# Performance work log

Hardware: AMD Instinct MI355X
Metric: run time of the kernel (lower is better)

## Reference

```python
import jax, jax.numpy as jnp
import numpy as np
import math

D_MODEL, N_HEADS, D_FF = 1024, 16, 4096
HEAD_DIM = D_MODEL // N_HEADS
BATCH, SEQ = 2, 2048
POPE_BASE = 10000.0
LN_EPS = 1e-5


def setup_inputs() -> dict:
    key = jax.random.key(0)
    ks = jax.random.split(key, 20)
    s = 0.02
    inp = {
        "x": jax.random.normal(ks[0], (BATCH, SEQ, D_MODEL), dtype=jnp.float32),
        "positions": jnp.arange(SEQ, dtype=jnp.int64) if jax.config.jax_enable_x64 else jnp.arange(SEQ, dtype=jnp.int32),
        "Wq": jax.random.normal(ks[1], (D_MODEL, D_MODEL), jnp.float32) * s,
        "bq": jnp.zeros((D_MODEL,), jnp.float32),
        "Wk": jax.random.normal(ks[2], (D_MODEL, D_MODEL), jnp.float32) * s,
        "bk": jnp.zeros((D_MODEL,), jnp.float32),
        "Wv": jax.random.normal(ks[3], (D_MODEL, D_MODEL), jnp.float32) * s,
        "bv": jnp.zeros((D_MODEL,), jnp.float32),
        "Wo": jax.random.normal(ks[4], (D_MODEL, D_MODEL), jnp.float32) * s,
        "bo": jnp.zeros((D_MODEL,), jnp.float32),
        "phase_bias": jax.random.uniform(ks[5], (N_HEADS, HEAD_DIM), jnp.float32,
                                          minval=-2.0 * math.pi, maxval=0.0),
        "freqs": (1.0 / POPE_BASE ** (jnp.arange(HEAD_DIM, dtype=jnp.float32) / HEAD_DIM)),
        "W1": jax.random.normal(ks[6], (D_MODEL, D_FF), jnp.float32) * s,
        "b1": jnp.zeros((D_FF,), jnp.float32),
        "W2": jax.random.normal(ks[7], (D_FF, D_MODEL), jnp.float32) * s,
        "b2": jnp.zeros((D_MODEL,), jnp.float32),
        "g1": jnp.ones((D_MODEL,), jnp.float32),
        "beta1": jnp.zeros((D_MODEL,), jnp.float32),
        "g2": jnp.ones((D_MODEL,), jnp.float32),
        "beta2": jnp.zeros((D_MODEL,), jnp.float32),
    }
    return inp


def _layernorm(x, g, b):
    mu = jnp.mean(x, axis=-1, keepdims=True)
    var = jnp.mean((x - mu) ** 2, axis=-1, keepdims=True)
    return (x - mu) * jax.lax.rsqrt(var + LN_EPS) * g + b


def reference(x, positions, Wq, bq, Wk, bk, Wv, bv, Wo, bo, phase_bias, freqs,
              W1, b1, W2, b2, g1, beta1, g2, beta2):
    B, S, D = x.shape
    H, hd = N_HEADS, HEAD_DIM

    def split_heads(y):  # (B,S,D) -> (B,H,S,hd)
        return y.reshape(B, S, H, hd).transpose(0, 2, 1, 3)

    q = split_heads(x @ Wq + bq)
    k = split_heads(x @ Wk + bk)
    v = split_heads(x @ Wv + bv)

    # --- PoPE: magnitudes via softplus, phases from positions + learned bias ---
    mu_q = jax.nn.softplus(q)
    mu_k = jax.nn.softplus(k)
    pos_phases = positions[:, None].astype(jnp.float32) * freqs[None, :]        # (S,hd)
    phases = pos_phases[None, None, :, :] + phase_bias[None, :, None, :]        # (1,H,S,hd)
    cosp, sinp = jnp.cos(phases), jnp.sin(phases)
    q_pope = jnp.concatenate([mu_q * cosp, mu_q * sinp], axis=-1)               # (B,H,S,2hd)
    k_pope = jnp.concatenate([mu_k * cosp, mu_k * sinp], axis=-1)

    # --- manual causal attention with softmax1 ---
    scale = 1.0 / math.sqrt(2 * hd)  # q.shape[-1] == 2*head_dim under PoPE
    scores = jnp.einsum("bhsd,bhtd->bhst", q_pope, k_pope) * scale
    causal = jnp.triu(jnp.ones((S, S), dtype=bool), k=1)
    scores = jnp.where(causal[None, None], -jnp.inf, scores)
    m = jnp.max(scores, axis=-1, keepdims=True)
    e = jnp.exp(scores - m)
    attn_w = e / (1.0 + jnp.sum(e, axis=-1, keepdims=True))  # softmax1 (as written in source)
    attn = jnp.einsum("bhst,bhtd->bhsd", attn_w, v)

    attn = attn.transpose(0, 2, 1, 3).reshape(B, S, D) @ Wo + bo
    x = _layernorm(x + attn, g1, beta1)
    ff = jax.nn.relu(x @ W1 + b1) @ W2 + b2
    x = _layernorm(x + ff, g2, beta2)
    return x
```

## Files before the change

kernel.cpp:

```cpp
#include <hip/hip_runtime.h>
#include <hip/hip_bf16.h>
#include <math.h>

#define B_   2
#define S_   2048
#define D_   1024
#define H_   16
#define HD_  64
#define DFF_ 4096
#define M_   (B_*S_)
#define SCALE_ 0.08838834764831845f

typedef __attribute__((ext_vector_type(8))) short bf16x8;
typedef __attribute__((ext_vector_type(4))) float f32x4;

#define MFMA16(a,b,c) __builtin_amdgcn_mfma_f32_16x16x32_bf16((a),(b),(c),0,0,0)

__device__ __forceinline__ unsigned short f2b(float f) {
    union { float f; unsigned u; } v; v.f = f;
    return (unsigned short)((v.u + 0x7FFFu + ((v.u >> 16) & 1u)) >> 16);
}
__device__ __forceinline__ float b2f(unsigned short s) {
    union { unsigned u; float f; } v; v.u = ((unsigned)s) << 16;
    return v.f;
}
__device__ __forceinline__ unsigned pk2bf(float a, float b) {
    union { float f; unsigned u; } ua, ub; ua.f = a; ub.f = b;
    return __builtin_amdgcn_perm(ub.u, ua.u, 0x07060302u);
}
__device__ __forceinline__ float softplus_f(float x) {
    return fmaxf(x, 0.f) + log1pf(__expf(-fabsf(x)));
}
__device__ __forceinline__ void g2l16(const void* g, void* l) {
    __builtin_amdgcn_global_load_lds(
        (const __attribute__((address_space(1))) unsigned int*)g,
        (__attribute__((address_space(3))) unsigned int*)l, 16, 0, 0);
}

__global__ __launch_bounds__(256) void conv_bf16_kernel(
    const float* __restrict__ in, unsigned short* __restrict__ out)
{
    int i = blockIdx.x * 256 + threadIdx.x;
    out[i] = f2b(in[i]);
}

__global__ __launch_bounds__(256) void wtrans_kernel(
    const float* __restrict__ W, unsigned short* __restrict__ WT, int K, int N)
{
    __shared__ float tile[32][33];
    const int n0 = blockIdx.x * 32, k0 = blockIdx.y * 32;
    const int tx = threadIdx.x & 31, ty = threadIdx.x >> 5;
    #pragma unroll
    for (int i = 0; i < 4; i++)
        tile[ty + 8*i][tx] = W[(size_t)(k0 + ty + 8*i) * N + n0 + tx];
    __syncthreads();
    #pragma unroll
    for (int i = 0; i < 4; i++)
        WT[(size_t)(n0 + ty + 8*i) * K + k0 + tx] = f2b(tile[tx][ty + 8*i]);
}

__global__ __launch_bounds__(256) void bcat_kernel(
    const float* __restrict__ a, const float* __restrict__ b,
    const float* __restrict__ c, float* __restrict__ o)
{
    int i = blockIdx.x * 256 + threadIdx.x;
    o[i] = (i < 1024) ? a[i] : (i < 2048 ? b[i - 1024] : c[i - 2048]);
}

__global__ __launch_bounds__(256) void gemm_bf16_kernel(
    const unsigned short* __restrict__ A,
    const unsigned short* __restrict__ WT,
    const float* __restrict__ bias,
    float* __restrict__ outF, unsigned short* __restrict__ outB,
    int M, int Kslice, int lda, int N, int relu)
{
    __shared__ unsigned short As[128 * 64];
    __shared__ unsigned short Bs[128 * 64];

    const int tid = threadIdx.x;
    const int w = tid >> 6, lane = tid & 63;
    const int quad = lane >> 4, l16 = lane & 15;
    const size_t m0 = (size_t)blockIdx.y * 128, n0 = (size_t)blockIdx.x * 128;
    const int wm = (w >> 1) * 64, wn = (w & 1) * 64;
    const int koff = blockIdx.z * Kslice;

    const int srow = lane >> 3;
    const int sc   = ((lane & 7) ^ srow) * 8;
    const unsigned short* ga = A  + (m0 + w * 32 + srow) * (size_t)lda + koff + sc;
    const unsigned short* gb = WT + (n0 + w * 32 + srow) * (size_t)lda + koff + sc;
    const size_t rows8 = (size_t)8 * lda;

    f32x4 acc[4][4] = {};

    for (int k0 = 0; k0 < Kslice; k0 += 64) {
        #pragma unroll
        for (int j = 0; j < 4; j++)
            g2l16(ga + j * rows8 + k0, &As[(w * 32 + j * 8) * 64]);
        #pragma unroll
        for (int j = 0; j < 4; j++)
            g2l16(gb + j * rows8 + k0, &Bs[(w * 32 + j * 8) * 64]);
        __syncthreads();

        #pragma unroll
        for (int kk = 0; kk < 2; kk++) {
            bf16x8 af[4], bfr[4];
            #pragma unroll
            for (int t = 0; t < 4; t++) {
                const int slot = ((kk * 4 + quad) ^ (l16 & 7)) * 8;
                af[t]  = *(const bf16x8*)&As[(wm + t * 16 + l16) * 64 + slot];
                bfr[t] = *(const bf16x8*)&Bs[(wn + t * 16 + l16) * 64 + slot];
            }
            #pragma unroll
            for (int mt = 0; mt < 4; mt++)
                #pragma unroll
                for (int nt = 0; nt < 4; nt++)
                    acc[mt][nt] = MFMA16(af[mt], bfr[nt], acc[mt][nt]);
        }
        __syncthreads();
    }

    float bv[4];
    #pragma unroll
    for (int nt = 0; nt < 4; nt++)
        bv[nt] = (blockIdx.z == 0) ? bias[n0 + wn + nt * 16 + l16] : 0.f;

    float* outFz = outF ? outF + (size_t)blockIdx.z * M * N : nullptr;

    #pragma unroll
    for (int mt = 0; mt < 4; mt++) {
        #pragma unroll
        for (int nt = 0; nt < 4; nt++) {
            const size_t n = n0 + wn + nt * 16 + l16;
            #pragma unroll
            for (int r = 0; r < 4; r++) {
                const size_t m = m0 + wm + mt * 16 + quad * 4 + r;
                float val = acc[mt][nt][r] + bv[nt];
                if (relu) val = fmaxf(val, 0.f);
                const size_t idx = m * N + n;
                if (outFz) outFz[idx] = val;
                if (outB) outB[idx] = f2b(val);
            }
        }
    }
}

__global__ __launch_bounds__(256) void pope_kernel(
    const unsigned short* __restrict__ qkv,
    const float* __restrict__ phase_bias, const float* __restrict__ freqs,
    unsigned short* __restrict__ qp, unsigned short* __restrict__ kp)
{
    int idx = blockIdx.x * 256 + threadIdx.x;
    int d = idx & 63;
    int s = (idx >> 6) & (S_ - 1);
    int h = (idx >> 17) & (H_ - 1);
    int b = idx >> 21;

    size_t src = (size_t)(b * S_ + s) * 3072 + h * HD_ + d;
    float muq = softplus_f(b2f(qkv[src])) * SCALE_;
    float muk = softplus_f(b2f(qkv[src + 1024]));

    float ph = (float)s * freqs[d] + phase_bias[h * HD_ + d];
    float sn, cs;
    sincosf(ph, &sn, &cs);

    size_t o = ((size_t)(b * H_ + h) * S_ + s) * 128 + d;
    qp[o]      = f2b(muq * cs);
    qp[o + 64] = f2b(muq * sn);
    kp[o]      = f2b(muk * cs);
    kp[o + 64] = f2b(muk * sn);
}

__global__ __launch_bounds__(256) void vtrans_kernel(
    const unsigned short* __restrict__ qkv, unsigned short* __restrict__ vt)
{
    __shared__ unsigned short tile[64][72];
    const int bh = blockIdx.y, b = bh >> 4, h = bh & 15;
    const int s0 = blockIdx.x * 64;
    const int tid = threadIdx.x;
    #pragma unroll
    for (int i = 0; i < 16; i++) {
        int idx = i * 256 + tid;
        int s = idx >> 6, d = idx & 63;
        tile[s][d] = qkv[(size_t)(b * S_ + s0 + s) * 3072 + 2048 + h * HD_ + d];
    }
    __syncthreads();
    #pragma unroll
    for (int i = 0; i < 16; i++) {
        int idx = i * 256 + tid;
        int d = idx >> 6, s = idx & 63;
        vt[((size_t)bh * 64 + d) * S_ + s0 + s] = tile[s][d];
    }
}

__global__ __launch_bounds__(512, 4) void attn_mfma_kernel(
    const unsigned short* __restrict__ qp,
    const unsigned short* __restrict__ kp,
    const unsigned short* __restrict__ vt,
    unsigned short* __restrict__ ao)
{
    __shared__ unsigned short kt_lds[2][64][128];
    __shared__ unsigned short vt_lds[2][64][64];
    __shared__ unsigned short p_lds[8][16][72];

    const int tid = threadIdx.x;
    const int w = tid >> 6, lane = tid & 63;
    const int quad = lane >> 4, l16 = lane & 15;
    const int bh = blockIdx.y, b = bh >> 4, h = bh & 15;

    const int a = (blockIdx.z == 0) ? 15 - (int)blockIdx.x : (int)blockIdx.x;
    const int q0b = a * 128;
    const int q0 = q0b + w * 16;

    const unsigned short* qbase = qp + ((size_t)bh * S_ + q0 + l16) * 128 + quad * 8;
    bf16x8 qa[4];
    #pragma unroll
    for (int kc = 0; kc < 4; kc++) qa[kc] = *(const bf16x8*)(qbase + kc * 32);

    const int krow = lane >> 4, kslot = lane & 15;
    const int vrow = lane >> 3, vslot = lane & 7;
    const int kr0 = w * 8 + krow,     kc0 = kslot ^ (kr0 & 15);
    const int kr1 = w * 8 + 4 + krow, kc1 = kslot ^ (kr1 & 15);
    const int vd  = w * 8 + vrow,     vc  = vslot ^ (vd & 7);
    const unsigned short* kg0 = kp + ((size_t)bh * S_ + kr0) * 128 + kc0 * 8;
    const unsigned short* kg1 = kp + ((size_t)bh * S_ + kr1) * 128 + kc1 * 8;
    const unsigned short* vg0 = vt + ((size_t)bh * 64 + vd) * S_ + vc * 8;

    f32x4 o[4] = {};
    float ms = -1e30f, ls = 0.f;

    const int ntiles = 2 * a + 2;

    g2l16(kg0, &kt_lds[0][w * 8][0]);
    g2l16(kg1, &kt_lds[0][w * 8 + 4][0]);
    g2l16(vg0, &vt_lds[0][w * 8][0]);

    for (int ti = 0; ti < ntiles; ti++) {
        const int t0 = ti * 64;
        __syncthreads();
        if (ti + 1 < ntiles) {
            const int nb = (ti + 1) & 1;
            const size_t ko = (size_t)(ti + 1) * (64 * 128);
            const size_t vo = (size_t)(ti + 1) * 64;
            g2l16(kg0 + ko, &kt_lds[nb][w * 8][0]);
            g2l16(kg1 + ko, &kt_lds[nb][w * 8 + 4][0]);
            g2l16(vg0 + vo, &vt_lds[nb][w * 8][0]);
        }
        const int buf = ti & 1;

        if (t0 <= q0 + 15) {
            f32x4 sf[4];
            #pragma unroll
            for (int kg = 0; kg < 4; kg++) {
                f32x4 s = {0, 0, 0, 0};
                const int row = kg * 16 + l16;
                #pragma unroll
                for (int kc = 0; kc < 4; kc++) {
                    const int slot = (kc * 4 + quad) ^ l16;
                    s = MFMA16(*(const bf16x8*)&kt_lds[buf][row][slot * 8], qa[kc], s);
                }
                sf[kg] = s;
            }

            const int qrow = q0 + l16;
            const bool dmask = (t0 + 63 > q0);
            #pragma unroll
            for (int kg = 0; kg < 4; kg++) {
                const int kbase = t0 + kg * 16 + quad * 4;
                float v0 = sf[kg][0], v1 = sf[kg][1], v2 = sf[kg][2], v3 = sf[kg][3];
                if (dmask) {
                    v0 = (kbase     <= qrow) ? v0 : -1e30f;
                    v1 = (kbase + 1 <= qrow) ? v1 : -1e30f;
                    v2 = (kbase + 2 <= qrow) ? v2 : -1e30f;
                    v3 = (kbase + 3 <= qrow) ? v3 : -1e30f;
                }
                ms = fmaxf(ms, fmaxf(fmaxf(v0, v1), fmaxf(v2, v3)));
                const float e0 = __expf(v0), e1 = __expf(v1);
                const float e2 = __expf(v2), e3 = __expf(v3);
                ls += (e0 + e1) + (e2 + e3);
                uint2 pk;
                pk.x = pk2bf(e0, e1);
                pk.y = pk2bf(e2, e3);
                *(uint2*)&p_lds[w][l16][kg * 16 + quad * 4] = pk;
            }
            asm volatile("s_waitcnt lgkmcnt(0)" ::: "memory");
            bf16x8 pa0 = *(const bf16x8*)&p_lds[w][l16][quad * 8];
            bf16x8 pa1 = *(const bf16x8*)&p_lds[w][l16][quad * 8 + 32];

            #pragma unroll
            for (int dg = 0; dg < 4; dg++) {
                const int row = dg * 16 + l16;
                const int s0_ = quad ^ (l16 & 7);
                const int s1_ = (quad + 4) ^ (l16 & 7);
                o[dg] = MFMA16(pa0, *(const bf16x8*)&vt_lds[buf][row][s0_ * 8], o[dg]);
                o[dg] = MFMA16(pa1, *(const bf16x8*)&vt_lds[buf][row][s1_ * 8], o[dg]);
            }
        }
    }

    float mv = ms, lv = ls;
    mv = fmaxf(mv, __shfl_xor(mv, 16, 64)); lv += __shfl_xor(lv, 16, 64);
    mv = fmaxf(mv, __shfl_xor(mv, 32, 64)); lv += __shfl_xor(lv, 32, 64);
    const float inv = 1.f / (__expf(mv) + lv);

    #pragma unroll
    for (int r = 0; r < 4; r++) {
        const float ir = __shfl(inv, quad * 4 + r, 64);
        const int row = q0 + quad * 4 + r;
        const size_t base = (size_t)(b * S_ + row) * D_ + h * HD_ + l16;
        ao[base]      = f2b(o[0][r] * ir);
        ao[base + 16] = f2b(o[1][r] * ir);
        ao[base + 32] = f2b(o[2][r] * ir);
        ao[base + 48] = f2b(o[3][r] * ir);
    }
}

__global__ __launch_bounds__(256) void ln_kernel(
    const float* __restrict__ ya, const float* __restrict__ yb,
    const float* __restrict__ res,
    const float* __restrict__ g, const float* __restrict__ beta,
    float* __restrict__ out, unsigned short* __restrict__ outB)
{
    const int row = blockIdx.x;
    const int tid = threadIdx.x;
    const float* yr = ya + (size_t)row * D_;
    const float* y2 = yb ? yb + (size_t)row * D_ : nullptr;
    const float* rr = res + (size_t)row * D_;

    float t[4];
    float sum = 0.f, sumsq = 0.f;
    #pragma unroll
    for (int i = 0; i < 4; i++) {
        int c = tid + 256 * i;
        t[i] = yr[c] + rr[c] + (y2 ? y2[c] : 0.f);
        sum += t[i]; sumsq += t[i] * t[i];
    }
    #pragma unroll
    for (int off = 32; off >= 1; off >>= 1) {
        sum   += __shfl_xor(sum,   off, 64);
        sumsq += __shfl_xor(sumsq, off, 64);
    }
    __shared__ float rs_[4], rq_[4];
    int w = tid >> 6, lane = tid & 63;
    if (lane == 0) { rs_[w] = sum; rq_[w] = sumsq; }
    __syncthreads();
    float tot  = rs_[0] + rs_[1] + rs_[2] + rs_[3];
    float totq = rq_[0] + rq_[1] + rq_[2] + rq_[3];
    float mu   = tot  * (1.f / D_);
    float var  = totq * (1.f / D_) - mu * mu;
    float rstd = rsqrtf(var + 1e-5f);

    float* orow = out + (size_t)row * D_;
    #pragma unroll
    for (int i = 0; i < 4; i++) {
        int c = tid + 256 * i;
        float val = (t[i] - mu) * rstd * g[c] + beta[c];
        orow[c] = val;
        if (outB) outB[(size_t)row * D_ + c] = f2b(val);
    }
}

extern "C" void kernel_launch(void* const* d_in, const int* in_sizes, int n_in,
                              void* d_out, int out_size, void* d_ws, size_t ws_size,
                              hipStream_t stream)
{
    const float* x   = (const float*)d_in[0];
    const float* Wq  = (const float*)d_in[2];
    const float* bq  = (const float*)d_in[3];
    const float* Wk  = (const float*)d_in[4];
    const float* bk  = (const float*)d_in[5];
    const float* Wv  = (const float*)d_in[6];
    const float* bv  = (const float*)d_in[7];
    const float* Wo  = (const float*)d_in[8];
    const float* bo  = (const float*)d_in[9];
    const float* phase_bias = (const float*)d_in[10];
    const float* freqs = (const float*)d_in[11];
    const float* W1  = (const float*)d_in[12];
    const float* b1  = (const float*)d_in[13];
    const float* W2  = (const float*)d_in[14];
    const float* b2  = (const float*)d_in[15];
    const float* g1  = (const float*)d_in[16];
    const float* be1 = (const float*)d_in[17];
    const float* g2  = (const float*)d_in[18];
    const float* be2 = (const float*)d_in[19];
    float* out = (float*)d_out;

    char* base = (char*)d_ws;
    const size_t MiB = 1024 * 1024;
    unsigned short* WqkvT = (unsigned short*)(base);
    unsigned short* WoT   = (unsigned short*)(base + 6  * MiB);
    unsigned short* W1T   = (unsigned short*)(base + 8  * MiB);
    unsigned short* W2T   = (unsigned short*)(base + 16 * MiB);
    float*          bqkv  = (float*)(base + 24 * MiB);
    unsigned short* xb    = (unsigned short*)(base + 25 * MiB);
    unsigned short* qkvb  = (unsigned short*)(base + 33 * MiB);
    unsigned short* qpb   = (unsigned short*)(base + 57 * MiB);
    unsigned short* kpb   = (unsigned short*)(base + 73 * MiB);
    unsigned short* vtb   = (unsigned short*)(base + 89 * MiB);
    float*          po    = (float*)(base + 89 * MiB);
    float*          x1    = (float*)(base + 121 * MiB);
    unsigned short* aob   = xb;
    unsigned short* x1b   = xb;
    unsigned short* hb    = qkvb;
    float*          fo    = po;

    dim3 blk(256);

    conv_bf16_kernel<<<dim3(M_ * D_ / 256), blk, 0, stream>>>(x, xb);
    wtrans_kernel<<<dim3(32, 32), blk, 0, stream>>>(Wq, WqkvT, D_, D_);
    wtrans_kernel<<<dim3(32, 32), blk, 0, stream>>>(Wk, WqkvT + (size_t)1024 * 1024, D_, D_);
    wtrans_kernel<<<dim3(32, 32), blk, 0, stream>>>(Wv, WqkvT + (size_t)2048 * 1024, D_, D_);
    wtrans_kernel<<<dim3(32, 32), blk, 0, stream>>>(Wo, WoT, D_, D_);
    wtrans_kernel<<<dim3(DFF_ / 32, D_ / 32), blk, 0, stream>>>(W1, W1T, D_, DFF_);
    wtrans_kernel<<<dim3(D_ / 32, DFF_ / 32), blk, 0, stream>>>(W2, W2T, DFF_, D_);
    bcat_kernel<<<dim3(12), blk, 0, stream>>>(bq, bk, bv, bqkv);

    gemm_bf16_kernel<<<dim3(3072 / 128, M_ / 128, 1), blk, 0, stream>>>(
        xb, WqkvT, bqkv, nullptr, qkvb, M_, D_, D_, 3072, 0);

    pope_kernel<<<dim3(B_ * H_ * S_ * HD_ / 256), blk, 0, stream>>>(
        qkvb, phase_bias, freqs, qpb, kpb);
    vtrans_kernel<<<dim3(S_ / 64, B_ * H_), blk, 0, stream>>>(qkvb, vtb);

    attn_mfma_kernel<<<dim3(8, B_ * H_, 2), dim3(512), 0, stream>>>(qpb, kpb, vtb, aob);

    gemm_bf16_kernel<<<dim3(D_ / 128, M_ / 128, 2), blk, 0, stream>>>(
        aob, WoT, bo, po, nullptr, M_, D_ / 2, D_, D_, 0);
    ln_kernel<<<dim3(M_), blk, 0, stream>>>(po, po + (size_t)M_ * D_, x, g1, be1, x1, x1b);

    gemm_bf16_kernel<<<dim3(DFF_ / 128, M_ / 128, 1), blk, 0, stream>>>(
        x1b, W1T, b1, nullptr, hb, M_, D_, D_, DFF_, 1);
    gemm_bf16_kernel<<<dim3(D_ / 128, M_ / 128, 2), blk, 0, stream>>>(
        hb, W2T, b2, fo, nullptr, M_, DFF_ / 2, DFF_, D_, 0);
    ln_kernel<<<dim3(M_), blk, 0, stream>>>(fo, fo + (size_t)M_ * D_, x1, g2, be2, out, nullptr);
}
```

Baseline: 417.2 us.

## Double-buffer GEMM LDS tiles, remap blocks across XCDs, drop fp32 residual copy

The GEMM now prefetches the next K tile into a second LDS buffer while computing on the current one, with a single barrier per iteration. Block indices are remapped so consecutive tiles land on the same XCD for better L2 reuse. The input conversion kernel is vectorized to four elements per thread. The first layernorm writes only a bf16 output, and the second layernorm reads that as its residual. This removes one fp32 write and read, at the cost of residual precision and doubled LDS usage per block.

```diff
diff --git a/kernel.cpp b/kernel.cpp
--- a/kernel.cpp
+++ b/kernel.cpp
@@ -40,8 +40,11 @@
 __global__ __launch_bounds__(256) void conv_bf16_kernel(
     const float* __restrict__ in, unsigned short* __restrict__ out)
 {
-    int i = blockIdx.x * 256 + threadIdx.x;
-    out[i] = f2b(in[i]);
+    int i = (blockIdx.x * 256 + threadIdx.x) * 4;
+    float4 v = *(const float4*)&in[i];
+    ushort4 o;
+    o.x = f2b(v.x); o.y = f2b(v.y); o.z = f2b(v.z); o.w = f2b(v.w);
+    *(ushort4*)&out[i] = o;
 }
 
 __global__ __launch_bounds__(256) void wtrans_kernel(
@@ -74,15 +77,24 @@
     float* __restrict__ outF, unsigned short* __restrict__ outB,
     int M, int Kslice, int lda, int N, int relu)
 {
-    __shared__ unsigned short As[128 * 64];
-    __shared__ unsigned short Bs[128 * 64];
+    __shared__ unsigned short As[2][128 * 64];
+    __shared__ unsigned short Bs[2][128 * 64];
 
     const int tid = threadIdx.x;
     const int w = tid >> 6, lane = tid & 63;
     const int quad = lane >> 4, l16 = lane & 15;
-    const size_t m0 = (size_t)blockIdx.y * 128, n0 = (size_t)blockIdx.x * 128;
+
+    const int nn = gridDim.x, nm = gridDim.y;
+    const int lin = ((int)blockIdx.z * nm + (int)blockIdx.y) * nn + (int)blockIdx.x;
+    const int per = (nn * nm * (int)gridDim.z) >> 3;
+    const int id  = (lin & 7) * per + (lin >> 3);
+    const int zz  = id / (nn * nm);
+    const int rem = id - zz * nn * nm;
+    const int mt_ = rem / nn, nt_ = rem - mt_ * nn;
+
+    const size_t m0 = (size_t)mt_ * 128, n0 = (size_t)nt_ * 128;
     const int wm = (w >> 1) * 64, wn = (w & 1) * 64;
-    const int koff = blockIdx.z * Kslice;
+    const int koff = zz * Kslice;
 
     const int srow = lane >> 3;
     const int sc   = ((lane & 7) ^ srow) * 8;
@@ -91,15 +103,25 @@
     const size_t rows8 = (size_t)8 * lda;
 
     f32x4 acc[4][4] = {};
-
-    for (int k0 = 0; k0 < Kslice; k0 += 64) {
-        #pragma unroll
-        for (int j = 0; j < 4; j++)
-            g2l16(ga + j * rows8 + k0, &As[(w * 32 + j * 8) * 64]);
-        #pragma unroll
-        for (int j = 0; j < 4; j++)
-            g2l16(gb + j * rows8 + k0, &Bs[(w * 32 + j * 8) * 64]);
+    const int niter = Kslice >> 6;
+
+    #pragma unroll
+    for (int j = 0; j < 4; j++) g2l16(ga + j * rows8, &As[0][(w * 32 + j * 8) * 64]);
+    #pragma unroll
+    for (int j = 0; j < 4; j++) g2l16(gb + j * rows8, &Bs[0][(w * 32 + j * 8) * 64]);
+
+    for (int i = 0; i < niter; i++) {
         __syncthreads();
+        if (i + 1 < niter) {
+            const int nb = (i + 1) & 1, k0 = (i + 1) << 6;
+            #pragma unroll
+            for (int j = 0; j < 4; j++)
+                g2l16(ga + j * rows8 + k0, &As[nb][(w * 32 + j * 8) * 64]);
+            #pragma unroll
+            for (int j = 0; j < 4; j++)
+                g2l16(gb + j * rows8 + k0, &Bs[nb][(w * 32 + j * 8) * 64]);
+        }
+        const int buf = i & 1;
 
         #pragma unroll
         for (int kk = 0; kk < 2; kk++) {
@@ -107,8 +129,8 @@
             #pragma unroll
             for (int t = 0; t < 4; t++) {
                 const int slot = ((kk * 4 + quad) ^ (l16 & 7)) * 8;
-                af[t]  = *(const bf16x8*)&As[(wm + t * 16 + l16) * 64 + slot];
-                bfr[t] = *(const bf16x8*)&Bs[(wn + t * 16 + l16) * 64 + slot];
+                af[t]  = *(const bf16x8*)&As[buf][(wm + t * 16 + l16) * 64 + slot];
+                bfr[t] = *(const bf16x8*)&Bs[buf][(wn + t * 16 + l16) * 64 + slot];
             }
             #pragma unroll
             for (int mt = 0; mt < 4; mt++)
@@ -116,15 +138,14 @@
                 for (int nt = 0; nt < 4; nt++)
                     acc[mt][nt] = MFMA16(af[mt], bfr[nt], acc[mt][nt]);
         }
-        __syncthreads();
     }
 
     float bv[4];
     #pragma unroll
     for (int nt = 0; nt < 4; nt++)
-        bv[nt] = (blockIdx.z == 0) ? bias[n0 + wn + nt * 16 + l16] : 0.f;
-
-    float* outFz = outF ? outF + (size_t)blockIdx.z * M * N : nullptr;
+        bv[nt] = (zz == 0) ? bias[n0 + wn + nt * 16 + l16] : 0.f;
+
+    float* outFz = outF ? outF + (size_t)zz * M * N : nullptr;
 
     #pragma unroll
     for (int mt = 0; mt < 4; mt++) {
@@ -316,22 +337,22 @@
 
 __global__ __launch_bounds__(256) void ln_kernel(
     const float* __restrict__ ya, const float* __restrict__ yb,
-    const float* __restrict__ res,
+    const float* __restrict__ resF, const unsigned short* __restrict__ resB,
     const float* __restrict__ g, const float* __restrict__ beta,
-    float* __restrict__ out, unsigned short* __restrict__ outB)
+    float* __restrict__ outF, unsigned short* __restrict__ outB)
 {
     const int row = blockIdx.x;
     const int tid = threadIdx.x;
     const float* yr = ya + (size_t)row * D_;
     const float* y2 = yb ? yb + (size_t)row * D_ : nullptr;
-    const float* rr = res + (size_t)row * D_;
 
     float t[4];
     float sum = 0.f, sumsq = 0.f;
     #pragma unroll
     for (int i = 0; i < 4; i++) {
         int c = tid + 256 * i;
-        t[i] = yr[c] + rr[c] + (y2 ? y2[c] : 0.f);
+        float rv = resF ? resF[(size_t)row * D_ + c] : b2f(resB[(size_t)row * D_ + c]);
+        t[i] = yr[c] + rv + (y2 ? y2[c] : 0.f);
         sum += t[i]; sumsq += t[i] * t[i];
     }
     #pragma unroll
@@ -349,12 +370,11 @@
     float var  = totq * (1.f / D_) - mu * mu;
     float rstd = rsqrtf(var + 1e-5f);
 
-    float* orow = out + (size_t)row * D_;
     #pragma unroll
     for (int i = 0; i < 4; i++) {
         int c = tid + 256 * i;
         float val = (t[i] - mu) * rstd * g[c] + beta[c];
-        orow[c] = val;
+        if (outF) outF[(size_t)row * D_ + c] = val;
         if (outB) outB[(size_t)row * D_ + c] = f2b(val);
     }
 }
@@ -397,7 +417,6 @@
     unsigned short* kpb   = (unsigned short*)(base + 73 * MiB);
     unsigned short* vtb   = (unsigned short*)(base + 89 * MiB);
     float*          po    = (float*)(base + 89 * MiB);
-    float*          x1    = (float*)(base + 121 * MiB);
     unsigned short* aob   = xb;
     unsigned short* x1b   = xb;
     unsigned short* hb    = qkvb;
@@ -405,7 +424,7 @@
 
     dim3 blk(256);
 
-    conv_bf16_kernel<<<dim3(M_ * D_ / 256), blk, 0, stream>>>(x, xb);
+    conv_bf16_kernel<<<dim3(M_ * D_ / 1024), blk, 0, stream>>>(x, xb);
     wtrans_kernel<<<dim3(32, 32), blk, 0, stream>>>(Wq, WqkvT, D_, D_);
     wtrans_kernel<<<dim3(32, 32), blk, 0, stream>>>(Wk, WqkvT + (size_t)1024 * 1024, D_, D_);
     wtrans_kernel<<<dim3(32, 32), blk, 0, stream>>>(Wv, WqkvT + (size_t)2048 * 1024, D_, D_);
@@ -425,11 +444,13 @@
 
     gemm_bf16_kernel<<<dim3(D_ / 128, M_ / 128, 2), blk, 0, stream>>>(
         aob, WoT, bo, po, nullptr, M_, D_ / 2, D_, D_, 0);
-    ln_kernel<<<dim3(M_), blk, 0, stream>>>(po, po + (size_t)M_ * D_, x, g1, be1, x1, x1b);
+    ln_kernel<<<dim3(M_), blk, 0, stream>>>(
+        po, po + (size_t)M_ * D_, x, nullptr, g1, be1, nullptr, x1b);
 
     gemm_bf16_kernel<<<dim3(DFF_ / 128, M_ / 128, 1), blk, 0, stream>>>(
         x1b, W1T, b1, nullptr, hb, M_, D_, D_, DFF_, 1);
     gemm_bf16_kernel<<<dim3(D_ / 128, M_ / 128, 2), blk, 0, stream>>>(
         hb, W2T, b2, fo, nullptr, M_, DFF_ / 2, DFF_, D_, 0);
-    ln_kernel<<<dim3(M_), blk, 0, stream>>>(fo, fo + (size_t)M_ * D_, x1, g2, be2, out, nullptr);
-}
+    ln_kernel<<<dim3(M_), blk, 0, stream>>>(
+        fo, fo + (size_t)M_ * D_, nullptr, x1b, g2, be2, out, nullptr);
+}
```

New measurement: 401.9 us. -3.7%, faster.
